# Kernel tuning notes

Hardware: AMD Instinct MI355X
Metric: run time of the kernel (lower is better)

Reference implementation:

```python
import jax, jax.numpy as jnp
import numpy as np


def euler2mat(omega):
    # omega: [3] Euler angles (x, y, z); R = Rz @ Ry @ Rx
    sx, sy, sz = jnp.sin(omega[0]), jnp.sin(omega[1]), jnp.sin(omega[2])
    cx, cy, cz = jnp.cos(omega[0]), jnp.cos(omega[1]), jnp.cos(omega[2])
    Rx = jnp.array([[1.0, 0.0, 0.0], [0.0, cx, -sx], [0.0, sx, cx]], dtype=omega.dtype)
    Ry = jnp.array([[cy, 0.0, sy], [0.0, 1.0, 0.0], [-sy, 0.0, cy]], dtype=omega.dtype)
    Rz = jnp.array([[cz, -sz, 0.0], [sz, cz, 0.0], [0.0, 0.0, 1.0]], dtype=omega.dtype)
    return Rz @ Ry @ Rx


def cd_loss(pred, gt):
    # pred: [N,3], gt: [K,3] -> mean over N of min_k ||pred_n - gt_k||^2
    a = jnp.sum(pred * pred, axis=1)[:, None]          # [N,1]
    b = jnp.sum(gt * gt, axis=1)[None, :]              # [1,K]
    c = jnp.einsum('ik,jk->ij', pred, gt)              # [N,K]
    dist = a + b - 2.0 * c                             # [N,K]
    return jnp.mean(jnp.min(dist, axis=1))


def setup_inputs() -> dict:
    key = jax.random.key(0)
    k1, k2, k3, k4 = jax.random.split(key, 4)
    return {
        "visual_points": jax.random.normal(k1, (16384, 3), dtype=jnp.float32),
        "tactile_points": jax.random.normal(k2, (2048, 3), dtype=jnp.float32),
        "model_points": jax.random.normal(k3, (8192, 3), dtype=jnp.float32),
        "scale": jnp.ones((), dtype=jnp.float32),
        "state": jax.random.normal(k4, (6,), dtype=jnp.float32),
    }


def reference(visual_points, tactile_points, model_points, scale, state):
    t = state[0:3]                 # translation [3]
    r = euler2mat(state[3:6])      # rotation [3,3]
    vc = ((visual_points - t[None, :]) @ r) / scale
    tc = ((tactile_points - t[None, :]) @ r) / scale
    E = 1.0 * cd_loss(vc, model_points) + 0.1 * cd_loss(tc, model_points)
    return E
```

## Files before the change

### kernel.cpp

```cpp
#include <hip/hip_runtime.h>
#include <hip/hip_bf16.h>

#define NVIS   16384
#define NTAC   2048
#define NPRED  (NVIS + NTAC)
#define NMODEL 8192

#define BLK    256
#define PPT    3
#define TILE   (BLK * PPT)
#define NTILE  (NPRED / TILE)
#define CHUNK  256
#define NCHUNK (NMODEL / CHUNK)

#define BIGF   3.4e38f


__global__ __launch_bounds__(BLK) void cd_transform_kernel(
    const float* __restrict__ vis,
    const float* __restrict__ tac,
    const float* __restrict__ model,
    const float* __restrict__ scale,
    const float* __restrict__ state,
    float4* __restrict__ pred4,
    float4* __restrict__ model4)
{
    const int tid = threadIdx.x;
    const int bid = blockIdx.x;

    if (bid < NPRED / BLK) {
        const float ax = state[3], ay = state[4], az = state[5];
        const float sx = sinf(ax), cx = cosf(ax);
        const float sy = sinf(ay), cy = cosf(ay);
        const float sz = sinf(az), cz = cosf(az);
        const float R00 = cz * cy;
        const float R01 = cz * sy * sx - sz * cx;
        const float R02 = cz * sy * cx + sz * sx;
        const float R10 = sz * cy;
        const float R11 = sz * sy * sx + cz * cx;
        const float R12 = sz * sy * cx - cz * sx;
        const float R20 = -sy;
        const float R21 = cy * sx;
        const float R22 = cy * cx;
        const float inv = 1.0f / scale[0];
        const float t0 = state[0], t1 = state[1], t2 = state[2];

        const int pid = bid * BLK + tid;
        const float* pp = (pid < NVIS) ? (vis + 3 * pid) : (tac + 3 * (pid - NVIS));
        const float p0 = pp[0] - t0;
        const float p1 = pp[1] - t1;
        const float p2 = pp[2] - t2;
        const float vx = (p0 * R00 + p1 * R10 + p2 * R20) * inv;
        const float vy = (p0 * R01 + p1 * R11 + p2 * R21) * inv;
        const float vz = (p0 * R02 + p1 * R12 + p2 * R22) * inv;
        pred4[pid] = make_float4(vx, vy, vz, vx * vx + vy * vy + vz * vz);
    } else {
        const int mid = (bid - NPRED / BLK) * BLK + tid;
        const float* mp = model + 3 * mid;
        const float mx = mp[0], my = mp[1], mz = mp[2];
        model4[mid] = make_float4(mx, my, mz, 0.5f * (mx * mx + my * my + mz * mz));
    }
}

__global__ __launch_bounds__(BLK) void cd_partial_kernel(
    const float4* __restrict__ pred4,
    const float4* __restrict__ model4,
    float* __restrict__ mins)
{
    __shared__ float4 sm[CHUNK];

    const int tid   = threadIdx.x;
    const int tile  = blockIdx.x;
    const int chunk = blockIdx.y;

    sm[tid] = model4[chunk * CHUNK + tid];

    float nx[PPT], ny[PPT], nz[PPT], pa[PPT];
    #pragma unroll
    for (int k = 0; k < PPT; ++k) {
        float4 p = pred4[tile * TILE + k * BLK + tid];
        nx[k] = -p.x; ny[k] = -p.y; nz[k] = -p.z; pa[k] = p.w;
    }

    __syncthreads();

    float b0 = BIGF, b1 = BIGF, b2 = BIGF;
    #pragma unroll 8
    for (int j = 0; j < CHUNK; ++j) {
        float4 m = sm[j];
        b0 = fminf(b0, fmaf(nx[0], m.x, fmaf(ny[0], m.y, fmaf(nz[0], m.z, m.w))));
        b1 = fminf(b1, fmaf(nx[1], m.x, fmaf(ny[1], m.y, fmaf(nz[1], m.z, m.w))));
        b2 = fminf(b2, fmaf(nx[2], m.x, fmaf(ny[2], m.y, fmaf(nz[2], m.z, m.w))));
    }

    float* mrow = mins + (size_t)chunk * NPRED + tile * TILE + tid;
    mrow[0 * BLK] = fmaf(2.0f, b0, pa[0]);
    mrow[1 * BLK] = fmaf(2.0f, b1, pa[1]);
    mrow[2 * BLK] = fmaf(2.0f, b2, pa[2]);
}

__global__ __launch_bounds__(BLK) void cd_reduce_kernel(
    const float* __restrict__ mins,
    float* __restrict__ out)
{
    const int tid = threadIdx.x;
    const int pid = blockIdx.x * BLK + tid;

    float b = mins[pid];
    #pragma unroll 8
    for (int c = 1; c < NCHUNK; ++c)
        b = fminf(b, mins[(size_t)c * NPRED + pid]);

    float v = b;
    #pragma unroll
    for (int off = 32; off > 0; off >>= 1)
        v += __shfl_down(v, off, 64);

    __shared__ float s[BLK / 64];
    if ((tid & 63) == 0) s[tid >> 6] = v;
    __syncthreads();

    if (tid == 0) {
        float t = s[0] + s[1] + s[2] + s[3];
        float scaled = (blockIdx.x < NVIS / BLK) ? t * (1.0f / (float)NVIS)
                                                 : t * (0.1f / (float)NTAC);
        atomicAdd(out, scaled);
    }
}

extern "C" void kernel_launch(void* const* d_in, const int* in_sizes, int n_in,
                              void* d_out, int out_size, void* d_ws, size_t ws_size,
                              hipStream_t stream) {
    const float* vis   = (const float*)d_in[0];
    const float* tac   = (const float*)d_in[1];
    const float* model = (const float*)d_in[2];
    const float* scale = (const float*)d_in[3];
    const float* state = (const float*)d_in[4];
    float* out = (float*)d_out;

    float4* pred4  = (float4*)d_ws;
    float4* model4 = pred4 + NPRED;
    float*  mins   = (float*)(model4 + NMODEL);

    hipMemsetAsync(out, 0, sizeof(float), stream);

    cd_transform_kernel<<<NPRED / BLK + NMODEL / BLK, BLK, 0, stream>>>(
        vis, tac, model, scale, state, pred4, model4);

    dim3 grid(NTILE, NCHUNK);
    cd_partial_kernel<<<grid, BLK, 0, stream>>>(pred4, model4, mins);
    cd_reduce_kernel<<<NPRED / BLK, BLK, 0, stream>>>(mins, out);
}
```

Measured before the change: 86.12 us.

## Transform model points into world frame and reduce per-point minima with atomicMin

Instead of rotating all 18432 query points into the model frame, the inverse transform is applied to the 8192 model points, and distances are rescaled by 1/scale^2 in the final reduction. The per-chunk minima buffer is replaced by atomicMin on float bit patterns into one array per point, which removes the large intermediate write and the chunk loop in the reduce kernel. The LDS staging of model points is also dropped in favour of direct global loads, which adds risk from uncached or non-broadcast load latency. The atomicMin on unsigned bits is correct only for non-negative values, and cancellation can make a distance slightly negative.

```diff
diff --git a/kernel.cpp b/kernel.cpp
--- a/kernel.cpp
+++ b/kernel.cpp
@@ -13,22 +13,22 @@
 #define CHUNK  256
 #define NCHUNK (NMODEL / CHUNK)
 
-#define BIGF   3.4e38f
+#define BIGF     3.4e38f
+#define INF_BITS 0x7F800000u
 
 
-__global__ __launch_bounds__(BLK) void cd_transform_kernel(
-    const float* __restrict__ vis,
-    const float* __restrict__ tac,
+
+__global__ __launch_bounds__(BLK) void cd_setup_kernel(
     const float* __restrict__ model,
     const float* __restrict__ scale,
     const float* __restrict__ state,
-    float4* __restrict__ pred4,
-    float4* __restrict__ model4)
+    float4* __restrict__ model4,
+    unsigned* __restrict__ pmin)
 {
     const int tid = threadIdx.x;
     const int bid = blockIdx.x;
 
-    if (bid < NPRED / BLK) {
+    if (bid < NMODEL / BLK) {
         const float ax = state[3], ay = state[4], az = state[5];
         const float sx = sinf(ax), cx = cosf(ax);
         const float sy = sinf(ay), cy = cosf(ay);
@@ -42,88 +42,82 @@
         const float R20 = -sy;
         const float R21 = cy * sx;
         const float R22 = cy * cx;
-        const float inv = 1.0f / scale[0];
         const float t0 = state[0], t1 = state[1], t2 = state[2];
+        const float s  = scale[0];
 
-        const int pid = bid * BLK + tid;
-        const float* pp = (pid < NVIS) ? (vis + 3 * pid) : (tac + 3 * (pid - NVIS));
-        const float p0 = pp[0] - t0;
-        const float p1 = pp[1] - t1;
-        const float p2 = pp[2] - t2;
-        const float vx = (p0 * R00 + p1 * R10 + p2 * R20) * inv;
-        const float vy = (p0 * R01 + p1 * R11 + p2 * R21) * inv;
-        const float vz = (p0 * R02 + p1 * R12 + p2 * R22) * inv;
-        pred4[pid] = make_float4(vx, vy, vz, vx * vx + vy * vy + vz * vz);
-    } else {
-        const int mid = (bid - NPRED / BLK) * BLK + tid;
+        const int mid = bid * BLK + tid;
         const float* mp = model + 3 * mid;
         const float mx = mp[0], my = mp[1], mz = mp[2];
-        model4[mid] = make_float4(mx, my, mz, 0.5f * (mx * mx + my * my + mz * mz));
+        const float wx = fmaf(s, mx * R00 + my * R01 + mz * R02, t0);
+        const float wy = fmaf(s, mx * R10 + my * R11 + mz * R12, t1);
+        const float wz = fmaf(s, mx * R20 + my * R21 + mz * R22, t2);
+        model4[mid] = make_float4(wx, wy, wz, 0.5f * (wx * wx + wy * wy + wz * wz));
+    } else {
+        const int pid = (bid - NMODEL / BLK) * BLK + tid;
+        pmin[pid] = INF_BITS;
     }
 }
 
 __global__ __launch_bounds__(BLK) void cd_partial_kernel(
-    const float4* __restrict__ pred4,
+    const float* __restrict__ vis,
+    const float* __restrict__ tac,
     const float4* __restrict__ model4,
-    float* __restrict__ mins)
+    unsigned* __restrict__ pmin)
 {
-    __shared__ float4 sm[CHUNK];
-
     const int tid   = threadIdx.x;
     const int tile  = blockIdx.x;
     const int chunk = blockIdx.y;
 
-    sm[tid] = model4[chunk * CHUNK + tid];
-
     float nx[PPT], ny[PPT], nz[PPT], pa[PPT];
     #pragma unroll
     for (int k = 0; k < PPT; ++k) {
-        float4 p = pred4[tile * TILE + k * BLK + tid];
-        nx[k] = -p.x; ny[k] = -p.y; nz[k] = -p.z; pa[k] = p.w;
+        const int pid = tile * TILE + k * BLK + tid;
+        const float* pp = (pid < NVIS) ? (vis + 3 * pid) : (tac + 3 * (pid - NVIS));
+        const float p0 = pp[0], p1 = pp[1], p2 = pp[2];
+        pa[k] = p0 * p0 + p1 * p1 + p2 * p2;
+        nx[k] = -p0; ny[k] = -p1; nz[k] = -p2;
     }
 
-    __syncthreads();
+    const float4* __restrict__ mrow = model4 + chunk * CHUNK;
 
     float b0 = BIGF, b1 = BIGF, b2 = BIGF;
     #pragma unroll 8
     for (int j = 0; j < CHUNK; ++j) {
-        float4 m = sm[j];
+        const float4 m = mrow[j];
         b0 = fminf(b0, fmaf(nx[0], m.x, fmaf(ny[0], m.y, fmaf(nz[0], m.z, m.w))));
         b1 = fminf(b1, fmaf(nx[1], m.x, fmaf(ny[1], m.y, fmaf(nz[1], m.z, m.w))));
         b2 = fminf(b2, fmaf(nx[2], m.x, fmaf(ny[2], m.y, fmaf(nz[2], m.z, m.w))));
     }
 
-    float* mrow = mins + (size_t)chunk * NPRED + tile * TILE + tid;
-    mrow[0 * BLK] = fmaf(2.0f, b0, pa[0]);
-    mrow[1 * BLK] = fmaf(2.0f, b1, pa[1]);
-    mrow[2 * BLK] = fmaf(2.0f, b2, pa[2]);
+    const int pbase = tile * TILE + tid;
+    atomicMin(&pmin[pbase + 0 * BLK], __float_as_uint(fmaf(2.0f, b0, pa[0])));
+    atomicMin(&pmin[pbase + 1 * BLK], __float_as_uint(fmaf(2.0f, b1, pa[1])));
+    atomicMin(&pmin[pbase + 2 * BLK], __float_as_uint(fmaf(2.0f, b2, pa[2])));
 }
 
 __global__ __launch_bounds__(BLK) void cd_reduce_kernel(
-    const float* __restrict__ mins,
+    const unsigned* __restrict__ pmin,
+    const float* __restrict__ scale,
     float* __restrict__ out)
 {
     const int tid = threadIdx.x;
     const int pid = blockIdx.x * BLK + tid;
 
-    float b = mins[pid];
-    #pragma unroll 8
-    for (int c = 1; c < NCHUNK; ++c)
-        b = fminf(b, mins[(size_t)c * NPRED + pid]);
-
-    float v = b;
+    float v = __uint_as_float(pmin[pid]);
     #pragma unroll
     for (int off = 32; off > 0; off >>= 1)
         v += __shfl_down(v, off, 64);
 
-    __shared__ float s[BLK / 64];
-    if ((tid & 63) == 0) s[tid >> 6] = v;
+    __shared__ float sh[BLK / 64];
+    if ((tid & 63) == 0) sh[tid >> 6] = v;
     __syncthreads();
 
     if (tid == 0) {
-        float t = s[0] + s[1] + s[2] + s[3];
-        float scaled = (blockIdx.x < NVIS / BLK) ? t * (1.0f / (float)NVIS)
-                                                 : t * (0.1f / (float)NTAC);
+        const float s = scale[0];
+        const float inv2 = 1.0f / (s * s);
+        const float t = sh[0] + sh[1] + sh[2] + sh[3];
+        const float scaled = (blockIdx.x < NVIS / BLK) ? t * inv2 * (1.0f / (float)NVIS)
+                                                       : t * inv2 * (0.1f / (float)NTAC);
         atomicAdd(out, scaled);
     }
 }
@@ -138,16 +132,16 @@
     const float* state = (const float*)d_in[4];
     float* out = (float*)d_out;
 
-    float4* pred4  = (float4*)d_ws;
-    float4* model4 = pred4 + NPRED;
-    float*  mins   = (float*)(model4 + NMODEL);
+    float4*   model4 = (float4*)d_ws;
+    unsigned* pmin   = (unsigned*)(model4 + NMODEL);
 
     hipMemsetAsync(out, 0, sizeof(float), stream);
 
-    cd_transform_kernel<<<NPRED / BLK + NMODEL / BLK, BLK, 0, stream>>>(
-        vis, tac, model, scale, state, pred4, model4);
+    cd_setup_kernel<<<NMODEL / BLK + NPRED / BLK, BLK, 0, stream>>>(
+        model, scale, state, model4, pmin);
 
     dim3 grid(NTILE, NCHUNK);
-    cd_partial_kernel<<<grid, BLK, 0, stream>>>(pred4, model4, mins);
-    cd_reduce_kernel<<<NPRED / BLK, BLK, 0, stream>>>(mins, out);
+    cd_partial_kernel<<<grid, BLK, 0, stream>>>(vis, tac, model4, pmin);
+
+    cd_reduce_kernel<<<NPRED / BLK, BLK, 0, stream>>>(pmin, scale, out);
 }
```

New measurement: 87.10 us. No clear change (+1.1%).
